# Optimization experiments

Measured on AMD Instinct MI355X. Metric: run time of the kernel, lower is better.

Reference implementation:

```python
import jax, jax.numpy as jnp
import numpy as np

N_EXC, N_INH = 4000, 1000
N = N_EXC + N_INH
DELAY = 15
TAU, DT = 20.0, 1.0
DECAY = 1.0 - DT / TAU  # 0.95 leaky-integration factor
V_TH, V_RESET = 1.0, 0.0
ALPHA = 4.0  # surrogate-gradient sharpness
CONN_P, J_W, G_INH = 0.1, 0.1, 5.0
T_STEPS, BATCH = 256, 8


@jax.custom_vjp
def spike_fn(x):
    return (x >= 0.0).astype(x.dtype)

def _spike_fwd(x):
    return spike_fn(x), x

def _spike_bwd(x, g):
    # sigmoid surrogate gradient: d/dx sigmoid(alpha*x)
    s = jax.nn.sigmoid(ALPHA * x)
    return (g * ALPHA * s * (1.0 - s),)

spike_fn.defvjp(_spike_fwd, _spike_bwd)


def setup_inputs() -> dict:
    key = jax.random.key(0)
    k1, k2 = jax.random.split(key, 2)
    # external drive (Poisson-like input current, positive mean)
    ext = jax.random.normal(k1, (T_STEPS, BATCH, N), dtype=jnp.float32) * 0.5 + 0.2
    # Brunel connectivity: prob CONN_P, exc cols weight +J, inh cols weight -g*J
    mask = (jax.random.uniform(k2, (N, N)) < CONN_P).astype(jnp.float32)
    col_w = jnp.concatenate([jnp.full((N_EXC,), J_W, jnp.float32),
                             jnp.full((N_INH,), -G_INH * J_W, jnp.float32)])
    W = mask * col_w[None, :]  # W[i, j] = weight from presyn j to postsyn i
    return {"external_input": ext, "W": W}


def reference(external_input, W):
    T, B, n = external_input.shape

    def step(carry, x_t):
        buf, v, idx = carry
        delayed = jax.lax.dynamic_index_in_dim(buf, idx, axis=0, keepdims=False)  # [B, N]
        i_total = delayed @ W.T + x_t                 # recurrent + external current
        v_new = v * DECAY + i_total                   # leaky integration
        s = spike_fn(v_new - V_TH)                    # threshold crossing
        v_out = (1.0 - s) * v_new + s * V_RESET       # hard reset
        buf = jax.lax.dynamic_update_index_in_dim(buf, s, idx, axis=0)
        return (buf, v_out, (idx + 1) % DELAY), (s, v_out)

    buf0 = jnp.zeros((DELAY, B, n), external_input.dtype)
    v0 = jnp.zeros((B, n), external_input.dtype)
    _, (spikes, vs) = jax.lax.scan(step, (buf0, v0, jnp.int32(0)), external_input)
    return spikes, vs
```

## Files before the change

### kernel.cpp

```cpp
#include <hip/hip_runtime.h>
#include <stdint.h>

#define NN      5000
#define NE      4000
#define NB      8
#define TSTEPS  256
#define NDELAY  15
#define NW      157
#define NIPAD   5120
#define RW      160
#define IPB     256
#define BPB     20
#define NBLK    (NB*BPB)
#define RING_SLOTS 32
#define CH      4
#define BARSTRIDE 16

#define MASK_BYTES (RW*NIPAD*4)
#define BAR_OFF    MASK_BYTES
#define BAR_BYTES  (64*BARSTRIDE*4)
#define RING_OFF   (BAR_OFF + BAR_BYTES)
#define RING_BYTES (RING_SLOTS*NB*RW*4)
#define ZERO_BYTES (RING_OFF + RING_BYTES)

__global__ void _Brunel_build_mask(const float* __restrict__ W,
                                   uint32_t* __restrict__ maskT2)
{
    int j = blockIdx.x * blockDim.x + threadIdx.x;
    int i = blockIdx.y;
    int lane = threadIdx.x & 63;
    bool nz = false;
    if (j < NN) nz = (W[(size_t)i * NN + j] != 0.0f);
    unsigned long long m = __ballot(nz);
    if ((lane & 31) == 0 && j < NN) {
        uint32_t wd = (lane == 0) ? (uint32_t)m : (uint32_t)(m >> 32);
        maskT2[(size_t)(j >> 5) * NIPAD + i] = wd;
    }
}

__global__ void __launch_bounds__(IPB, 1) _Brunel_persist(
    const float* __restrict__ ext,
    const uint32_t* __restrict__ maskT2,
    uint32_t* __restrict__ ring,
    int* __restrict__ barc,
    float* __restrict__ out_spk,
    float* __restrict__ out_vs)
{
    const int tx   = threadIdx.x;
    const int bb   = blockIdx.x;
    const int b    = bb / BPB;
    const int i    = (bb % BPB) * IPB + tx;
    const bool act = (i < NN);
    const int lane = tx & 63;

    __shared__ __align__(16) uint32_t s_mask[IPB][156];
    __shared__ uint32_t s_mask156[IPB];
    __shared__ __align__(16) uint32_t s_spk[CH][RW];

    for (int w = 0; w < NW; ++w) {
        uint32_t mv = maskT2[(size_t)w * NIPAD + i];
        if (w < 156) s_mask[tx][w] = mv; else s_mask156[tx] = mv;
    }
    for (int idx = tx; idx < CH * RW; idx += IPB)
        ((uint32_t*)s_spk)[idx] = 0u;
    __syncthreads();

    float v = 0.0f;

    for (int t0 = 0, m = 0; t0 < TSTEPS; t0 += CH, ++m) {
        float x0 = 0.f, x1 = 0.f, x2 = 0.f, x3 = 0.f;
        if (act) {
            const float* e0 = ext + ((size_t)t0 * NB + b) * NN + i;
            const size_t st = (size_t)NB * NN;
            x0 = e0[0]; x1 = e0[st]; x2 = e0[2 * st]; x3 = e0[3 * st];
        }

        if (m >= 3) {
            if (tx == 0) {
                const int* c3 = barc + (size_t)(m - 3) * BARSTRIDE;
                while (__hip_atomic_load(c3, __ATOMIC_RELAXED,
                                         __HIP_MEMORY_SCOPE_AGENT) < NBLK)
                    __builtin_amdgcn_s_sleep(2);
            }
            __syncthreads();
            const int ts0 = t0 - NDELAY;
            for (int it = 0; it < (CH * RW + IPB - 1) / IPB; ++it) {
                int idx = tx + it * IPB;
                if (idx < CH * RW) {
                    int k = idx / RW, w = idx - k * RW;
                    int ts = ts0 + k;
                    ((uint32_t*)s_spk)[idx] = __hip_atomic_load(
                        &ring[((size_t)(ts & (RING_SLOTS - 1)) * NB + b) * RW + w],
                        __ATOMIC_RELAXED, __HIP_MEMORY_SCOPE_AGENT);
                }
            }
            __syncthreads();
        }

        int cE0 = 0, cE1 = 0, cE2 = 0, cE3 = 0;
        int cI0 = 0, cI1 = 0, cI2 = 0, cI3 = 0;
        const uint32_t* __restrict__ mrow = s_mask[tx];

#pragma unroll 4
        for (int c = 0; c < 31; ++c) {
            uint4 m4 = *(const uint4*)(mrow + 4 * c);
            uint4 a0 = *(const uint4*)(&s_spk[0][4 * c]);
            uint4 a1 = *(const uint4*)(&s_spk[1][4 * c]);
            uint4 a2 = *(const uint4*)(&s_spk[2][4 * c]);
            uint4 a3 = *(const uint4*)(&s_spk[3][4 * c]);
            cE0 += __popc(m4.x & a0.x) + __popc(m4.y & a0.y)
                 + __popc(m4.z & a0.z) + __popc(m4.w & a0.w);
            cE1 += __popc(m4.x & a1.x) + __popc(m4.y & a1.y)
                 + __popc(m4.z & a1.z) + __popc(m4.w & a1.w);
            cE2 += __popc(m4.x & a2.x) + __popc(m4.y & a2.y)
                 + __popc(m4.z & a2.z) + __popc(m4.w & a2.w);
            cE3 += __popc(m4.x & a3.x) + __popc(m4.y & a3.y)
                 + __popc(m4.z & a3.z) + __popc(m4.w & a3.w);
        }
        {
            uint4 m4 = *(const uint4*)(mrow + 124);
            uint4 a0 = *(const uint4*)(&s_spk[0][124]);
            uint4 a1 = *(const uint4*)(&s_spk[1][124]);
            uint4 a2 = *(const uint4*)(&s_spk[2][124]);
            uint4 a3 = *(const uint4*)(&s_spk[3][124]);
            cE0 += __popc(m4.x & a0.x);
            cI0 += __popc(m4.y & a0.y) + __popc(m4.z & a0.z) + __popc(m4.w & a0.w);
            cE1 += __popc(m4.x & a1.x);
            cI1 += __popc(m4.y & a1.y) + __popc(m4.z & a1.z) + __popc(m4.w & a1.w);
            cE2 += __popc(m4.x & a2.x);
            cI2 += __popc(m4.y & a2.y) + __popc(m4.z & a2.z) + __popc(m4.w & a2.w);
            cE3 += __popc(m4.x & a3.x);
            cI3 += __popc(m4.y & a3.y) + __popc(m4.z & a3.z) + __popc(m4.w & a3.w);
        }
#pragma unroll 4
        for (int c = 32; c < 39; ++c) {
            uint4 m4 = *(const uint4*)(mrow + 4 * c);
            uint4 a0 = *(const uint4*)(&s_spk[0][4 * c]);
            uint4 a1 = *(const uint4*)(&s_spk[1][4 * c]);
            uint4 a2 = *(const uint4*)(&s_spk[2][4 * c]);
            uint4 a3 = *(const uint4*)(&s_spk[3][4 * c]);
            cI0 += __popc(m4.x & a0.x) + __popc(m4.y & a0.y)
                 + __popc(m4.z & a0.z) + __popc(m4.w & a0.w);
            cI1 += __popc(m4.x & a1.x) + __popc(m4.y & a1.y)
                 + __popc(m4.z & a1.z) + __popc(m4.w & a1.w);
            cI2 += __popc(m4.x & a2.x) + __popc(m4.y & a2.y)
                 + __popc(m4.z & a2.z) + __popc(m4.w & a2.w);
            cI3 += __popc(m4.x & a3.x) + __popc(m4.y & a3.y)
                 + __popc(m4.z & a3.z) + __popc(m4.w & a3.w);
        }
        {
            uint32_t mL = s_mask156[tx];
            cI0 += __popc(mL & s_spk[0][156]);
            cI1 += __popc(mL & s_spk[1][156]);
            cI2 += __popc(mL & s_spk[2][156]);
            cI3 += __popc(mL & s_spk[3][156]);
        }

#define BRUNEL_STEP(kk, xk)                                                   \
        {                                                                     \
            const int t = t0 + kk;                                            \
            float cur = 0.1f * (float)cE##kk - 0.5f * (float)cI##kk;          \
            v = v * 0.95f + (cur + xk);                                       \
            bool s = act && (v >= 1.0f);                                      \
            float sflag = s ? 1.0f : 0.0f;                                    \
            float vout  = s ? 0.0f : v;                                       \
            if (act) {                                                        \
                size_t o = ((size_t)t * NB + b) * NN + i;                     \
                out_spk[o] = sflag;                                           \
                out_vs[o]  = vout;                                            \
            }                                                                 \
            v = vout;                                                         \
            unsigned long long bm = __ballot(s);                              \
            if ((lane & 31) == 0 && act) {                                    \
                uint32_t wd = (lane == 0) ? (uint32_t)bm : (uint32_t)(bm >> 32); \
                __hip_atomic_store(                                           \
                    &ring[((size_t)(t & (RING_SLOTS - 1)) * NB + b) * RW + (i >> 5)], \
                    wd, __ATOMIC_RELAXED, __HIP_MEMORY_SCOPE_AGENT);          \
            }                                                                 \
        }
        BRUNEL_STEP(0, x0)
        BRUNEL_STEP(1, x1)
        BRUNEL_STEP(2, x2)
        BRUNEL_STEP(3, x3)
#undef BRUNEL_STEP

        asm volatile("s_waitcnt vmcnt(0)" ::: "memory");
        __syncthreads();
        if (tx == 0)
            __hip_atomic_fetch_add(barc + (size_t)m * BARSTRIDE, 1,
                                   __ATOMIC_RELAXED, __HIP_MEMORY_SCOPE_AGENT);
    }
}

extern "C" void kernel_launch(void* const* d_in, const int* in_sizes, int n_in,
                              void* d_out, int out_size, void* d_ws, size_t ws_size,
                              hipStream_t stream)
{
    const float* ext = (const float*)d_in[0];
    const float* W   = (const float*)d_in[1];

    float* out_spk = (float*)d_out;
    float* out_vs  = out_spk + (size_t)TSTEPS * NB * NN;

    uint8_t*  ws   = (uint8_t*)d_ws;
    uint32_t* mask = (uint32_t*)(ws);
    int*      barc = (int*)(ws + BAR_OFF);
    uint32_t* ring = (uint32_t*)(ws + RING_OFF);

    hipMemsetAsync(ws, 0, ZERO_BYTES, stream);

    dim3 gmask(NIPAD / IPB, NN);
    _Brunel_build_mask<<<gmask, IPB, 0, stream>>>(W, mask);

    _Brunel_persist<<<NBLK, IPB, 0, stream>>>(ext, mask, ring, barc,
                                              out_spk, out_vs);
}
```

Baseline: 475.9 us.

## Split each neuron's popcount reduction across two threads per neuron

Each block now runs 512 threads, with two lanes per postsynaptic neuron. Each lane handles half of the mask words, and the partial counts are combined with a shuffle. The inhibitory count is computed separately on a tail range, and the excitatory count is recovered as the total minus the inhibitory count. Spike ballots are compacted to the even lanes, so one 32-bit ring word is written per wave. This is meant to halve the serial popcount loop length in the latency-bound per-step critical path, at the cost of more threads, redundant work on the odd lanes, and some divergence.

```diff
diff --git a/kernel.cpp b/kernel.cpp
--- a/kernel.cpp
+++ b/kernel.cpp
@@ -9,9 +9,9 @@
 #define NW      157
 #define NIPAD   5120
 #define RW      160
-#define IPB     256
-#define BPB     20
-#define NBLK    (NB*BPB)
+#define IPB     512
+#define NSL     20
+#define NBLK    (NB*NSL)
 #define RING_SLOTS 32
 #define CH      4
 #define BARSTRIDE 16
@@ -38,7 +38,18 @@
     }
 }
 
-__global__ void __launch_bounds__(IPB, 1) _Brunel_persist(
+__device__ __forceinline__ uint32_t compress_even(unsigned long long bm)
+{
+    bm &= 0x5555555555555555ull;
+    bm = (bm | (bm >> 1))  & 0x3333333333333333ull;
+    bm = (bm | (bm >> 2))  & 0x0F0F0F0F0F0F0F0Full;
+    bm = (bm | (bm >> 4))  & 0x00FF00FF00FF00FFull;
+    bm = (bm | (bm >> 8))  & 0x0000FFFF0000FFFFull;
+    bm = (bm | (bm >> 16));
+    return (uint32_t)bm;
+}
+
+__global__ void __launch_bounds__(IPB, 2) _Brunel_persist(
     const float* __restrict__ ext,
     const uint32_t* __restrict__ maskT2,
     uint32_t* __restrict__ ring,
@@ -47,25 +58,34 @@
     float* __restrict__ out_vs)
 {
     const int tx   = threadIdx.x;
+    const int wv   = tx >> 6;
+    const int lane = tx & 63;
+    const int nl   = tx >> 1;
+    const int q    = tx & 1;
     const int bb   = blockIdx.x;
-    const int b    = bb / BPB;
-    const int i    = (bb % BPB) * IPB + tx;
+    const int b    = bb / NSL;
+    const int sl   = bb % NSL;
+    const int i    = sl * 256 + nl;
     const bool act = (i < NN);
-    const int lane = tx & 63;
-
-    __shared__ __align__(16) uint32_t s_mask[IPB][156];
-    __shared__ uint32_t s_mask156[IPB];
+
+    __shared__ __align__(16) uint32_t s_mask[256][156];
+    __shared__ uint32_t s_mask156[256];
     __shared__ __align__(16) uint32_t s_spk[CH][RW];
 
-    for (int w = 0; w < NW; ++w) {
-        uint32_t mv = maskT2[(size_t)w * NIPAD + i];
-        if (w < 156) s_mask[tx][w] = mv; else s_mask156[tx] = mv;
+    for (int c = 0; c < 79; ++c) {
+        int w = 2 * c + q;
+        if (w < NW) {
+            uint32_t mv = maskT2[(size_t)w * NIPAD + i];
+            if (w < 156) s_mask[nl][w] = mv;
+            else         s_mask156[nl] = mv;
+        }
     }
     for (int idx = tx; idx < CH * RW; idx += IPB)
         ((uint32_t*)s_spk)[idx] = 0u;
     __syncthreads();
 
     float v = 0.0f;
+    const int wbase = 80 * q;
 
     for (int t0 = 0, m = 0; t0 < TSTEPS; t0 += CH, ++m) {
         float x0 = 0.f, x1 = 0.f, x2 = 0.f, x3 = 0.f;
@@ -84,7 +104,7 @@
             }
             __syncthreads();
             const int ts0 = t0 - NDELAY;
-            for (int it = 0; it < (CH * RW + IPB - 1) / IPB; ++it) {
+            for (int it = 0; it < 2; ++it) {
                 int idx = tx + it * IPB;
                 if (idx < CH * RW) {
                     int k = idx / RW, w = idx - k * RW;
@@ -97,85 +117,78 @@
             __syncthreads();
         }
 
-        int cE0 = 0, cE1 = 0, cE2 = 0, cE3 = 0;
-        int cI0 = 0, cI1 = 0, cI2 = 0, cI3 = 0;
-        const uint32_t* __restrict__ mrow = s_mask[tx];
-
+        int S0 = 0, S1 = 0, S2 = 0, S3 = 0;
+        int V0 = 0, V1 = 0, V2 = 0, V3 = 0;
+        const uint32_t* __restrict__ mrow = s_mask[nl];
 #pragma unroll 4
-        for (int c = 0; c < 31; ++c) {
-            uint4 m4 = *(const uint4*)(mrow + 4 * c);
-            uint4 a0 = *(const uint4*)(&s_spk[0][4 * c]);
-            uint4 a1 = *(const uint4*)(&s_spk[1][4 * c]);
-            uint4 a2 = *(const uint4*)(&s_spk[2][4 * c]);
-            uint4 a3 = *(const uint4*)(&s_spk[3][4 * c]);
-            cE0 += __popc(m4.x & a0.x) + __popc(m4.y & a0.y)
-                 + __popc(m4.z & a0.z) + __popc(m4.w & a0.w);
-            cE1 += __popc(m4.x & a1.x) + __popc(m4.y & a1.y)
-                 + __popc(m4.z & a1.z) + __popc(m4.w & a1.w);
-            cE2 += __popc(m4.x & a2.x) + __popc(m4.y & a2.y)
-                 + __popc(m4.z & a2.z) + __popc(m4.w & a2.w);
-            cE3 += __popc(m4.x & a3.x) + __popc(m4.y & a3.y)
-                 + __popc(m4.z & a3.z) + __popc(m4.w & a3.w);
+        for (int c = 0; c < 20; ++c) {
+            int w0 = wbase + 4 * c;
+            if (w0 < 156) {
+                uint4 m4 = *(const uint4*)(mrow + w0);
+                uint4 a0 = *(const uint4*)(&s_spk[0][w0]);
+                uint4 a1 = *(const uint4*)(&s_spk[1][w0]);
+                uint4 a2 = *(const uint4*)(&s_spk[2][w0]);
+                uint4 a3 = *(const uint4*)(&s_spk[3][w0]);
+                S0 += __popc(m4.x & a0.x) + __popc(m4.y & a0.y)
+                    + __popc(m4.z & a0.z) + __popc(m4.w & a0.w);
+                S1 += __popc(m4.x & a1.x) + __popc(m4.y & a1.y)
+                    + __popc(m4.z & a1.z) + __popc(m4.w & a1.w);
+                S2 += __popc(m4.x & a2.x) + __popc(m4.y & a2.y)
+                    + __popc(m4.z & a2.z) + __popc(m4.w & a2.w);
+                S3 += __popc(m4.x & a3.x) + __popc(m4.y & a3.y)
+                    + __popc(m4.z & a3.z) + __popc(m4.w & a3.w);
+            }
+        }
+#pragma unroll 4
+        for (int ww = 0; ww < 16; ++ww) {
+            int w = 125 + 16 * q + ww;
+            if (w < 156) {
+                uint32_t mw = mrow[w];
+                V0 += __popc(mw & s_spk[0][w]);
+                V1 += __popc(mw & s_spk[1][w]);
+                V2 += __popc(mw & s_spk[2][w]);
+                V3 += __popc(mw & s_spk[3][w]);
+            }
         }
         {
-            uint4 m4 = *(const uint4*)(mrow + 124);
-            uint4 a0 = *(const uint4*)(&s_spk[0][124]);
-            uint4 a1 = *(const uint4*)(&s_spk[1][124]);
-            uint4 a2 = *(const uint4*)(&s_spk[2][124]);
-            uint4 a3 = *(const uint4*)(&s_spk[3][124]);
-            cE0 += __popc(m4.x & a0.x);
-            cI0 += __popc(m4.y & a0.y) + __popc(m4.z & a0.z) + __popc(m4.w & a0.w);
-            cE1 += __popc(m4.x & a1.x);
-            cI1 += __popc(m4.y & a1.y) + __popc(m4.z & a1.z) + __popc(m4.w & a1.w);
-            cE2 += __popc(m4.x & a2.x);
-            cI2 += __popc(m4.y & a2.y) + __popc(m4.z & a2.z) + __popc(m4.w & a2.w);
-            cE3 += __popc(m4.x & a3.x);
-            cI3 += __popc(m4.y & a3.y) + __popc(m4.z & a3.z) + __popc(m4.w & a3.w);
-        }
-#pragma unroll 4
-        for (int c = 32; c < 39; ++c) {
-            uint4 m4 = *(const uint4*)(mrow + 4 * c);
-            uint4 a0 = *(const uint4*)(&s_spk[0][4 * c]);
-            uint4 a1 = *(const uint4*)(&s_spk[1][4 * c]);
-            uint4 a2 = *(const uint4*)(&s_spk[2][4 * c]);
-            uint4 a3 = *(const uint4*)(&s_spk[3][4 * c]);
-            cI0 += __popc(m4.x & a0.x) + __popc(m4.y & a0.y)
-                 + __popc(m4.z & a0.z) + __popc(m4.w & a0.w);
-            cI1 += __popc(m4.x & a1.x) + __popc(m4.y & a1.y)
-                 + __popc(m4.z & a1.z) + __popc(m4.w & a1.w);
-            cI2 += __popc(m4.x & a2.x) + __popc(m4.y & a2.y)
-                 + __popc(m4.z & a2.z) + __popc(m4.w & a2.w);
-            cI3 += __popc(m4.x & a3.x) + __popc(m4.y & a3.y)
-                 + __popc(m4.z & a3.z) + __popc(m4.w & a3.w);
-        }
-        {
-            uint32_t mL = s_mask156[tx];
-            cI0 += __popc(mL & s_spk[0][156]);
-            cI1 += __popc(mL & s_spk[1][156]);
-            cI2 += __popc(mL & s_spk[2][156]);
-            cI3 += __popc(mL & s_spk[3][156]);
-        }
+            uint32_t m156 = s_mask156[nl];
+            int p0 = __popc(m156 & s_spk[0][156]);
+            int p1 = __popc(m156 & s_spk[1][156]);
+            int p2 = __popc(m156 & s_spk[2][156]);
+            int p3 = __popc(m156 & s_spk[3][156]);
+            if (q == 0) {
+                S0 += p0; S1 += p1; S2 += p2; S3 += p3;
+                V0 += p0; V1 += p1; V2 += p2; V3 += p3;
+            }
+        }
+        S0 += __shfl_xor(S0, 1); S1 += __shfl_xor(S1, 1);
+        S2 += __shfl_xor(S2, 1); S3 += __shfl_xor(S3, 1);
+        V0 += __shfl_xor(V0, 1); V1 += __shfl_xor(V1, 1);
+        V2 += __shfl_xor(V2, 1); V3 += __shfl_xor(V3, 1);
 
 #define BRUNEL_STEP(kk, xk)                                                   \
         {                                                                     \
             const int t = t0 + kk;                                            \
-            float cur = 0.1f * (float)cE##kk - 0.5f * (float)cI##kk;          \
+            int cI = V##kk;                                                   \
+            int cE = S##kk - V##kk;                                           \
+            float cur = 0.1f * (float)cE - 0.5f * (float)cI;                  \
             v = v * 0.95f + (cur + xk);                                       \
             bool s = act && (v >= 1.0f);                                      \
             float sflag = s ? 1.0f : 0.0f;                                    \
             float vout  = s ? 0.0f : v;                                       \
-            if (act) {                                                        \
+            if (act && q == 0) {                                              \
                 size_t o = ((size_t)t * NB + b) * NN + i;                     \
                 out_spk[o] = sflag;                                           \
                 out_vs[o]  = vout;                                            \
             }                                                                 \
             v = vout;                                                         \
             unsigned long long bm = __ballot(s);                              \
-            if ((lane & 31) == 0 && act) {                                    \
-                uint32_t wd = (lane == 0) ? (uint32_t)bm : (uint32_t)(bm >> 32); \
+            uint32_t wbits = compress_even(bm);                               \
+            if (lane == 0) {                                                  \
                 __hip_atomic_store(                                           \
-                    &ring[((size_t)(t & (RING_SLOTS - 1)) * NB + b) * RW + (i >> 5)], \
-                    wd, __ATOMIC_RELAXED, __HIP_MEMORY_SCOPE_AGENT);          \
+                    &ring[((size_t)(t & (RING_SLOTS - 1)) * NB + b) * RW      \
+                          + sl * 8 + wv],                                     \
+                    wbits, __ATOMIC_RELAXED, __HIP_MEMORY_SCOPE_AGENT);       \
             }                                                                 \
         }
         BRUNEL_STEP(0, x0)
@@ -209,8 +222,8 @@
 
     hipMemsetAsync(ws, 0, ZERO_BYTES, stream);
 
-    dim3 gmask(NIPAD / IPB, NN);
-    _Brunel_build_mask<<<gmask, IPB, 0, stream>>>(W, mask);
+    dim3 gmask(NIPAD / 256, NN);
+    _Brunel_build_mask<<<gmask, 256, 0, stream>>>(W, mask);
 
     _Brunel_persist<<<NBLK, IPB, 0, stream>>>(ext, mask, ring, barc,
                                               out_spk, out_vs);
```

Result: slower. 529.6 us (+11.3%).

## Prefetch next chunk's delayed spikes into registers before computing current chunk

Applied to the files above, without the earlier changes.

The persistent kernel now waits on the grid barrier for chunk m-2 and loads the next chunk's delayed spike words from the ring into registers (one 64-bit load plus an optional 32-bit load per thread). These are written to shared memory at the start of the following chunk, so the global ring load latency overlaps with the popcount work of the current chunk instead of sitting on the critical path. The cost is waiting on the barrier one chunk earlier, which tightens the slack between blocks given the 15-step delay and 4-step chunks. One __syncthreads per chunk is also removed.

```diff
diff --git a/kernel.cpp b/kernel.cpp
--- a/kernel.cpp
+++ b/kernel.cpp
@@ -2,7 +2,6 @@
 #include <stdint.h>
 
 #define NN      5000
-#define NE      4000
 #define NB      8
 #define TSTEPS  256
 #define NDELAY  15
@@ -14,6 +13,7 @@
 #define NBLK    (NB*BPB)
 #define RING_SLOTS 32
 #define CH      4
+#define NCHUNK  (TSTEPS/CH)
 #define BARSTRIDE 16
 
 #define MASK_BYTES (RW*NIPAD*4)
@@ -56,16 +56,18 @@
     __shared__ __align__(16) uint32_t s_mask[IPB][156];
     __shared__ uint32_t s_mask156[IPB];
     __shared__ __align__(16) uint32_t s_spk[CH][RW];
+    uint32_t* s_flat = (uint32_t*)s_spk;
 
     for (int w = 0; w < NW; ++w) {
         uint32_t mv = maskT2[(size_t)w * NIPAD + i];
         if (w < 156) s_mask[tx][w] = mv; else s_mask156[tx] = mv;
     }
-    for (int idx = tx; idx < CH * RW; idx += IPB)
-        ((uint32_t*)s_spk)[idx] = 0u;
+    for (int idx = tx; idx < CH * RW; idx += IPB) s_flat[idx] = 0u;
     __syncthreads();
 
     float v = 0.0f;
+    uint64_t rAB = 0;
+    uint32_t rC  = 0;
 
     for (int t0 = 0, m = 0; t0 < TSTEPS; t0 += CH, ++m) {
         float x0 = 0.f, x1 = 0.f, x2 = 0.f, x3 = 0.f;
@@ -76,25 +78,35 @@
         }
 
         if (m >= 3) {
+            ((uint64_t*)s_flat)[tx] = rAB;
+            if (tx < CH * RW - 2 * IPB) s_flat[2 * IPB + tx] = rC;
+            __syncthreads();
+        }
+
+        if (m >= 2 && m < NCHUNK - 1) {
             if (tx == 0) {
-                const int* c3 = barc + (size_t)(m - 3) * BARSTRIDE;
+                const int* c3 = barc + (size_t)(m - 2) * BARSTRIDE;
                 while (__hip_atomic_load(c3, __ATOMIC_RELAXED,
                                          __HIP_MEMORY_SCOPE_AGENT) < NBLK)
                     __builtin_amdgcn_s_sleep(2);
             }
             __syncthreads();
-            const int ts0 = t0 - NDELAY;
-            for (int it = 0; it < (CH * RW + IPB - 1) / IPB; ++it) {
-                int idx = tx + it * IPB;
-                if (idx < CH * RW) {
-                    int k = idx / RW, w = idx - k * RW;
-                    int ts = ts0 + k;
-                    ((uint32_t*)s_spk)[idx] = __hip_atomic_load(
-                        &ring[((size_t)(ts & (RING_SLOTS - 1)) * NB + b) * RW + w],
-                        __ATOMIC_RELAXED, __HIP_MEMORY_SCOPE_AGENT);
-                }
+            const int ts0 = (t0 + CH) - NDELAY;
+            {
+                const int f = 2 * tx, k = f / RW, w = f - k * RW;
+                const int ts = ts0 + k;
+                const uint64_t* src = (const uint64_t*)
+                    &ring[((size_t)(ts & (RING_SLOTS - 1)) * NB + b) * RW + w];
+                rAB = __hip_atomic_load(src, __ATOMIC_RELAXED,
+                                        __HIP_MEMORY_SCOPE_AGENT);
             }
-            __syncthreads();
+            if (tx < CH * RW - 2 * IPB) {
+                const int f = 2 * IPB + tx, k = f / RW, w = f - k * RW;
+                const int ts = ts0 + k;
+                rC = __hip_atomic_load(
+                    &ring[((size_t)(ts & (RING_SLOTS - 1)) * NB + b) * RW + w],
+                    __ATOMIC_RELAXED, __HIP_MEMORY_SCOPE_AGENT);
+            }
         }
 
         int cE0 = 0, cE1 = 0, cE2 = 0, cE3 = 0;
```

Result: no change. 482.6 us (+1.4%).

## Prefetch delayed spike words into registers one chunk ahead and broadcast via readlane

Applied to the files above, without the earlier changes.

Drops the shared-memory spike staging buffer and its second block barrier. Each lane now loads ring words for the next chunk into VGPRs one chunk in advance, so the ring read latency overlaps the current chunk's popcount work. During the popcount loop the spike words are broadcast with readlane, which turns them into scalar operands instead of LDS reads. The barrier wait index shifts to m-2 to match the earlier prefetch, which tightens the schedule relative to the delay and raises register pressure through a fully unrolled loop.

```diff
diff --git a/kernel.cpp b/kernel.cpp
--- a/kernel.cpp
+++ b/kernel.cpp
@@ -2,7 +2,6 @@
 #include <stdint.h>
 
 #define NN      5000
-#define NE      4000
 #define NB      8
 #define TSTEPS  256
 #define NDELAY  15
@@ -14,6 +13,7 @@
 #define NBLK    (NB*BPB)
 #define RING_SLOTS 32
 #define CH      4
+#define NCHUNK  (TSTEPS/CH)
 #define BARSTRIDE 16
 
 #define MASK_BYTES (RW*NIPAD*4)
@@ -55,19 +55,28 @@
 
     __shared__ __align__(16) uint32_t s_mask[IPB][156];
     __shared__ uint32_t s_mask156[IPB];
-    __shared__ __align__(16) uint32_t s_spk[CH][RW];
 
     for (int w = 0; w < NW; ++w) {
         uint32_t mv = maskT2[(size_t)w * NIPAD + i];
         if (w < 156) s_mask[tx][w] = mv; else s_mask156[tx] = mv;
     }
-    for (int idx = tx; idx < CH * RW; idx += IPB)
-        ((uint32_t*)s_spk)[idx] = 0u;
     __syncthreads();
 
     float v = 0.0f;
 
+    uint32_t cA0=0,cA1=0,cA2=0, cB0=0,cB1=0,cB2=0,
+             cC0=0,cC1=0,cC2=0, cD0=0,cD1=0,cD2=0;
+    uint32_t nA0=0,nA1=0,nA2=0, nB0=0,nB1=0,nB2=0,
+             nC0=0,nC1=0,nC2=0, nD0=0,nD1=0,nD2=0;
+
+    const int wg0 = lane;
+    const int wg1 = 64 + lane;
+    const int wg2 = (128 + lane > 156) ? 156 : 128 + lane;
+
     for (int t0 = 0, m = 0; t0 < TSTEPS; t0 += CH, ++m) {
+        cA0=nA0; cA1=nA1; cA2=nA2; cB0=nB0; cB1=nB1; cB2=nB2;
+        cC0=nC0; cC1=nC1; cC2=nC2; cD0=nD0; cD1=nD1; cD2=nD2;
+
         float x0 = 0.f, x1 = 0.f, x2 = 0.f, x3 = 0.f;
         if (act) {
             const float* e0 = ext + ((size_t)t0 * NB + b) * NN + i;
@@ -75,86 +84,78 @@
             x0 = e0[0]; x1 = e0[st]; x2 = e0[2 * st]; x3 = e0[3 * st];
         }
 
-        if (m >= 3) {
+        if (m >= 2 && m < NCHUNK - 1) {
             if (tx == 0) {
-                const int* c3 = barc + (size_t)(m - 3) * BARSTRIDE;
+                const int* c3 = barc + (size_t)(m - 2) * BARSTRIDE;
                 while (__hip_atomic_load(c3, __ATOMIC_RELAXED,
                                          __HIP_MEMORY_SCOPE_AGENT) < NBLK)
                     __builtin_amdgcn_s_sleep(2);
             }
             __syncthreads();
-            const int ts0 = t0 - NDELAY;
-            for (int it = 0; it < (CH * RW + IPB - 1) / IPB; ++it) {
-                int idx = tx + it * IPB;
-                if (idx < CH * RW) {
-                    int k = idx / RW, w = idx - k * RW;
-                    int ts = ts0 + k;
-                    ((uint32_t*)s_spk)[idx] = __hip_atomic_load(
-                        &ring[((size_t)(ts & (RING_SLOTS - 1)) * NB + b) * RW + w],
-                        __ATOMIC_RELAXED, __HIP_MEMORY_SCOPE_AGENT);
-                }
-            }
-            __syncthreads();
+            const int ts0 = (t0 + CH) - NDELAY;
+#define RLD(KOFF, WRD) __hip_atomic_load(                                     \
+        &ring[((size_t)(((ts0 + (KOFF)) & (RING_SLOTS - 1)) * NB + b)) * RW   \
+              + (WRD)], __ATOMIC_RELAXED, __HIP_MEMORY_SCOPE_AGENT)
+            nA0 = RLD(0, wg0); nA1 = RLD(0, wg1); nA2 = RLD(0, wg2);
+            nB0 = RLD(1, wg0); nB1 = RLD(1, wg1); nB2 = RLD(1, wg2);
+            nC0 = RLD(2, wg0); nC1 = RLD(2, wg1); nC2 = RLD(2, wg2);
+            nD0 = RLD(3, wg0); nD1 = RLD(3, wg1); nD2 = RLD(3, wg2);
+#undef RLD
         }
 
         int cE0 = 0, cE1 = 0, cE2 = 0, cE3 = 0;
         int cI0 = 0, cI1 = 0, cI2 = 0, cI3 = 0;
         const uint32_t* __restrict__ mrow = s_mask[tx];
 
-#pragma unroll 4
-        for (int c = 0; c < 31; ++c) {
-            uint4 m4 = *(const uint4*)(mrow + 4 * c);
-            uint4 a0 = *(const uint4*)(&s_spk[0][4 * c]);
-            uint4 a1 = *(const uint4*)(&s_spk[1][4 * c]);
-            uint4 a2 = *(const uint4*)(&s_spk[2][4 * c]);
-            uint4 a3 = *(const uint4*)(&s_spk[3][4 * c]);
-            cE0 += __popc(m4.x & a0.x) + __popc(m4.y & a0.y)
-                 + __popc(m4.z & a0.z) + __popc(m4.w & a0.w);
-            cE1 += __popc(m4.x & a1.x) + __popc(m4.y & a1.y)
-                 + __popc(m4.z & a1.z) + __popc(m4.w & a1.w);
-            cE2 += __popc(m4.x & a2.x) + __popc(m4.y & a2.y)
-                 + __popc(m4.z & a2.z) + __popc(m4.w & a2.w);
-            cE3 += __popc(m4.x & a3.x) + __popc(m4.y & a3.y)
-                 + __popc(m4.z & a3.z) + __popc(m4.w & a3.w);
-        }
-        {
-            uint4 m4 = *(const uint4*)(mrow + 124);
-            uint4 a0 = *(const uint4*)(&s_spk[0][124]);
-            uint4 a1 = *(const uint4*)(&s_spk[1][124]);
-            uint4 a2 = *(const uint4*)(&s_spk[2][124]);
-            uint4 a3 = *(const uint4*)(&s_spk[3][124]);
-            cE0 += __popc(m4.x & a0.x);
-            cI0 += __popc(m4.y & a0.y) + __popc(m4.z & a0.z) + __popc(m4.w & a0.w);
-            cE1 += __popc(m4.x & a1.x);
-            cI1 += __popc(m4.y & a1.y) + __popc(m4.z & a1.z) + __popc(m4.w & a1.w);
-            cE2 += __popc(m4.x & a2.x);
-            cI2 += __popc(m4.y & a2.y) + __popc(m4.z & a2.z) + __popc(m4.w & a2.w);
-            cE3 += __popc(m4.x & a3.x);
-            cI3 += __popc(m4.y & a3.y) + __popc(m4.z & a3.z) + __popc(m4.w & a3.w);
-        }
-#pragma unroll 4
-        for (int c = 32; c < 39; ++c) {
-            uint4 m4 = *(const uint4*)(mrow + 4 * c);
-            uint4 a0 = *(const uint4*)(&s_spk[0][4 * c]);
-            uint4 a1 = *(const uint4*)(&s_spk[1][4 * c]);
-            uint4 a2 = *(const uint4*)(&s_spk[2][4 * c]);
-            uint4 a3 = *(const uint4*)(&s_spk[3][4 * c]);
-            cI0 += __popc(m4.x & a0.x) + __popc(m4.y & a0.y)
-                 + __popc(m4.z & a0.z) + __popc(m4.w & a0.w);
-            cI1 += __popc(m4.x & a1.x) + __popc(m4.y & a1.y)
-                 + __popc(m4.z & a1.z) + __popc(m4.w & a1.w);
-            cI2 += __popc(m4.x & a2.x) + __popc(m4.y & a2.y)
-                 + __popc(m4.z & a2.z) + __popc(m4.w & a2.w);
-            cI3 += __popc(m4.x & a3.x) + __popc(m4.y & a3.y)
-                 + __popc(m4.z & a3.z) + __popc(m4.w & a3.w);
-        }
+#define PROC(MW, W, LN, SA, SB, SC, SD)                                       \
+        { uint32_t u0 = (uint32_t)__builtin_amdgcn_readlane((int)(SA), (LN)); \
+          uint32_t u1 = (uint32_t)__builtin_amdgcn_readlane((int)(SB), (LN)); \
+          uint32_t u2 = (uint32_t)__builtin_amdgcn_readlane((int)(SC), (LN)); \
+          uint32_t u3 = (uint32_t)__builtin_amdgcn_readlane((int)(SD), (LN)); \
+          if ((W) < 125) {                                                    \
+              cE0 += __popc((MW) & u0); cE1 += __popc((MW) & u1);             \
+              cE2 += __popc((MW) & u2); cE3 += __popc((MW) & u3);             \
+          } else {                                                            \
+              cI0 += __popc((MW) & u0); cI1 += __popc((MW) & u1);             \
+              cI2 += __popc((MW) & u2); cI3 += __popc((MW) & u3);             \
+          } }
+
+#define GRP(G, L, SA, SB, SC, SD)                                             \
+        { uint4 m4 = *(const uint4*)(mrow + 64 * (G) + 4 * (L));              \
+          PROC(m4.x, 64*(G)+4*(L)+0, 4*(L)+0, SA, SB, SC, SD)                 \
+          PROC(m4.y, 64*(G)+4*(L)+1, 4*(L)+1, SA, SB, SC, SD)                 \
+          PROC(m4.z, 64*(G)+4*(L)+2, 4*(L)+2, SA, SB, SC, SD)                 \
+          PROC(m4.w, 64*(G)+4*(L)+3, 4*(L)+3, SA, SB, SC, SD) }
+
+        GRP(0, 0,cA0,cB0,cC0,cD0) GRP(0, 1,cA0,cB0,cC0,cD0)
+        GRP(0, 2,cA0,cB0,cC0,cD0) GRP(0, 3,cA0,cB0,cC0,cD0)
+        GRP(0, 4,cA0,cB0,cC0,cD0) GRP(0, 5,cA0,cB0,cC0,cD0)
+        GRP(0, 6,cA0,cB0,cC0,cD0) GRP(0, 7,cA0,cB0,cC0,cD0)
+        GRP(0, 8,cA0,cB0,cC0,cD0) GRP(0, 9,cA0,cB0,cC0,cD0)
+        GRP(0,10,cA0,cB0,cC0,cD0) GRP(0,11,cA0,cB0,cC0,cD0)
+        GRP(0,12,cA0,cB0,cC0,cD0) GRP(0,13,cA0,cB0,cC0,cD0)
+        GRP(0,14,cA0,cB0,cC0,cD0) GRP(0,15,cA0,cB0,cC0,cD0)
+        GRP(1, 0,cA1,cB1,cC1,cD1) GRP(1, 1,cA1,cB1,cC1,cD1)
+        GRP(1, 2,cA1,cB1,cC1,cD1) GRP(1, 3,cA1,cB1,cC1,cD1)
+        GRP(1, 4,cA1,cB1,cC1,cD1) GRP(1, 5,cA1,cB1,cC1,cD1)
+        GRP(1, 6,cA1,cB1,cC1,cD1) GRP(1, 7,cA1,cB1,cC1,cD1)
+        GRP(1, 8,cA1,cB1,cC1,cD1) GRP(1, 9,cA1,cB1,cC1,cD1)
+        GRP(1,10,cA1,cB1,cC1,cD1) GRP(1,11,cA1,cB1,cC1,cD1)
+        GRP(1,12,cA1,cB1,cC1,cD1) GRP(1,13,cA1,cB1,cC1,cD1)
+        GRP(1,14,cA1,cB1,cC1,cD1) GRP(1,15,cA1,cB1,cC1,cD1)
+        GRP(2, 0,cA2,cB2,cC2,cD2) GRP(2, 1,cA2,cB2,cC2,cD2)
+        GRP(2, 2,cA2,cB2,cC2,cD2) GRP(2, 3,cA2,cB2,cC2,cD2)
+        GRP(2, 4,cA2,cB2,cC2,cD2) GRP(2, 5,cA2,cB2,cC2,cD2)
+        GRP(2, 6,cA2,cB2,cC2,cD2)
         {
             uint32_t mL = s_mask156[tx];
-            cI0 += __popc(mL & s_spk[0][156]);
-            cI1 += __popc(mL & s_spk[1][156]);
-            cI2 += __popc(mL & s_spk[2][156]);
-            cI3 += __popc(mL & s_spk[3][156]);
-        }
+            cI0 += __popc(mL & (uint32_t)__builtin_amdgcn_readlane((int)cA2, 28));
+            cI1 += __popc(mL & (uint32_t)__builtin_amdgcn_readlane((int)cB2, 28));
+            cI2 += __popc(mL & (uint32_t)__builtin_amdgcn_readlane((int)cC2, 28));
+            cI3 += __popc(mL & (uint32_t)__builtin_amdgcn_readlane((int)cD2, 28));
+        }
+#undef GRP
+#undef PROC
 
 #define BRUNEL_STEP(kk, xk)                                                   \
         {                                                                     \
```

New measurement: 601.0 us. 26.3% more time.
